# Kernel tuning notes

Measured on AMD Instinct MI355X. Metric: run time of the kernel, lower is better.

Reference implementation:

```python
import jax, jax.numpy as jnp
import numpy as np

HIDDEN = 128
GRID = 8
NB = 32.0            # neighborhood_size
CELL = NB / GRID      # cell_size


def setup_inputs() -> dict:
    key = jax.random.key(0)
    k1, k2, k3, k4 = jax.random.split(key, 4)
    N = 1024
    hidden_states = jax.random.normal(k1, (N, HIDDEN), dtype=jnp.float32)
    positions = jax.random.uniform(k2, (N, 2), dtype=jnp.float32) * 100.0
    fan_in = GRID * GRID * HIDDEN
    bound = 1.0 / np.sqrt(fan_in)
    W = jax.random.uniform(k3, (fan_in, HIDDEN), dtype=jnp.float32, minval=-bound, maxval=bound)
    b = jax.random.uniform(k4, (HIDDEN,), dtype=jnp.float32, minval=-bound, maxval=bound)
    return {"hidden_states": hidden_states, "positions": positions, "W": W, "b": b}


def reference(hidden_states, positions, W, b):
    N, H = hidden_states.shape
    G = GRID
    pos = jax.lax.stop_gradient(positions)  # indices carry no gradient (matches torch int())
    # rel[i, j] = positions[j] - positions[i]
    rel = pos[None, :, :] - pos[:, None, :]                      # [N, N, 2]
    half = NB / 2.0
    inside = (jnp.abs(rel[..., 0]) <= half) & (jnp.abs(rel[..., 1]) <= half)
    not_self = ~jnp.eye(N, dtype=bool)
    valid = inside & not_self                                     # [N, N]
    # rel + half is in [0, NB] when inside, so floor == int() truncation
    gx = jnp.clip(jnp.floor((rel[..., 0] + half) / CELL).astype(jnp.int32), 0, G - 1)
    gy = jnp.clip(jnp.floor((rel[..., 1] + half) / CELL).astype(jnp.int32), 0, G - 1)
    cell = gy * G + gx                                            # [N, N], in [0, G*G)
    # invalid pairs go to a dummy cell G*G per pedestrian
    seg = jnp.where(valid, cell, G * G)
    gid = (jnp.arange(N, dtype=jnp.int32)[:, None] * (G * G + 1) + seg).reshape(-1)
    data = jnp.broadcast_to(hidden_states[None, :, :], (N, N, H)).reshape(N * N, H)
    gmax = jax.ops.segment_max(data, gid, num_segments=N * (G * G + 1))  # [N*(G*G+1), H]
    # torch grid starts at zeros and uses maximum -> clamp at 0; empty cells (-inf) -> 0
    grid = jnp.maximum(gmax.reshape(N, G * G + 1, H)[:, : G * G, :], 0.0)  # [N, G*G, H]
    flat = grid.reshape(N, G * G * H)
    return flat @ W + b
```

## Files before the change

### kernel.cpp

```cpp
#include <hip/hip_runtime.h>
#include <hip/hip_bf16.h>

#define N_PED 1024
#define H 128
#define G 8
#define NCELL 64
#define K_TOT 8192
#define HALF_NB 16.0f
#define INV_CELL 0.25f

#define KSPLIT 16
#define KC 512
#define BM 32
#define BK 64
#define NSTAGE 8

typedef __attribute__((ext_vector_type(8))) short bf16x8;
typedef __attribute__((ext_vector_type(4))) float f32x4;

__device__ __forceinline__ unsigned map_f2u(float v) {
    unsigned u = __float_as_uint(v);
    return (u & 0x80000000u) ? ~u : (u | 0x80000000u);
}
__device__ __forceinline__ float unmap_u2f(unsigned u) {
    return __uint_as_float((u & 0x80000000u) ? (u ^ 0x80000000u) : ~u);
}
__device__ __forceinline__ unsigned pack2(unsigned ua, unsigned ub) {
    float2 f = {unmap_u2f(ua), unmap_u2f(ub)};
    union { __hip_bfloat162 h; unsigned u; } cv;
    cv.h = __float22bfloat162_rn(f);
    return cv.u;
}
__device__ __forceinline__ unsigned pack2f(float fa, float fb) {
    float2 f = {fa, fb};
    union { __hip_bfloat162 h; unsigned u; } cv;
    cv.h = __float22bfloat162_rn(f);
    return cv.u;
}
__device__ __forceinline__ void gl_lds16(const void* g, void* l) {
    __builtin_amdgcn_global_load_lds(
        (const __attribute__((address_space(1))) void*)g,
        (__attribute__((address_space(3))) void*)l, 16, 0, 0);
}

__global__ __launch_bounds__(512) void fused_pre(const float* __restrict__ hs,
                                                 const float* __restrict__ pos,
                                                 const float* __restrict__ W,
                                                 const float* __restrict__ b,
                                                 ushort* __restrict__ grid,
                                                 ushort* __restrict__ Wt,
                                                 float* __restrict__ out) {
    __shared__ __align__(16) char smem[36872];
    const int tid = threadIdx.x;

    if (blockIdx.x < N_PED) {
        unsigned* lgrid = (unsigned*)smem;
        int*      list  = (int*)(smem + 32768);
        int*      cnt   = (int*)(smem + 36864);
        const int i = blockIdx.x;

        const unsigned iu = 0x80000000u;
        uint4 iv = {iu, iu, iu, iu};
        for (int k = tid; k < NCELL * H / 4; k += 512) ((uint4*)lgrid)[k] = iv;
        if (tid == 0) *cnt = 0;
        __syncthreads();

        const float2 pi = ((const float2*)pos)[i];
        for (int j = tid; j < N_PED; j += 512) {
            float2 pj = ((const float2*)pos)[j];
            float rx = pj.x - pi.x;
            float ry = pj.y - pi.y;
            if (j != i && fabsf(rx) <= HALF_NB && fabsf(ry) <= HALF_NB) {
                int gx = min(G - 1, max(0, (int)floorf((rx + HALF_NB) * INV_CELL)));
                int gy = min(G - 1, max(0, (int)floorf((ry + HALF_NB) * INV_CELL)));
                int slot = atomicAdd(cnt, 1);
                list[slot] = (j << 8) | (gy * G + gx);
            }
        }
        __syncthreads();

        const int n  = *cnt;
        const int c  = tid & 31;
        const int eg = tid >> 5;
        int e  = eg;
        int p0 = (e < n) ? list[e] : -1;
        int p1 = (e + 16 < n) ? list[e + 16] : -1;
        float v0[4] = {};
        if (p0 >= 0) {
            const float* hp = &hs[(p0 >> 8) * H + c];
            v0[0] = hp[0]; v0[1] = hp[32]; v0[2] = hp[64]; v0[3] = hp[96];
        }
        while (p0 >= 0) {
            int p2 = (e + 32 < n) ? list[e + 32] : -1;
            float v1[4] = {};
            if (p1 >= 0) {
                const float* hp = &hs[(p1 >> 8) * H + c];
                v1[0] = hp[0]; v1[1] = hp[32]; v1[2] = hp[64]; v1[3] = hp[96];
            }
            unsigned* gph = &lgrid[(p0 & 255) * H + c];
            atomicMax(gph + 0,  map_f2u(v0[0]));
            atomicMax(gph + 32, map_f2u(v0[1]));
            atomicMax(gph + 64, map_f2u(v0[2]));
            atomicMax(gph + 96, map_f2u(v0[3]));
            e += 16; p0 = p1; p1 = p2;
            v0[0] = v1[0]; v0[1] = v1[1]; v0[2] = v1[2]; v0[3] = v1[3];
        }
        __syncthreads();

        uint4* dst = (uint4*)(grid + (size_t)i * K_TOT);
        for (int q = tid; q < K_TOT / 8; q += 512) {
            uint4 a  = ((const uint4*)lgrid)[2 * q];
            uint4 bq = ((const uint4*)lgrid)[2 * q + 1];
            uint4 o;
            o.x = pack2(a.x,  a.y);
            o.y = pack2(a.z,  a.w);
            o.z = pack2(bq.x, bq.y);
            o.w = pack2(bq.z, bq.w);
            dst[q] = o;
        }
    } else if (blockIdx.x < N_PED + 128) {
        float* tile = (float*)smem;
        const int bw  = blockIdx.x - N_PED;
        const int k0w = bw * 64;

        for (int x = tid; x < 64 * H; x += 512) {
            int r = x >> 7, cc = x & 127;
            tile[r * 129 + cc] = W[(size_t)(k0w + r) * H + cc];
        }
        __syncthreads();

        const int col = tid >> 2;
        const int kh  = (tid & 3) * 16;
        uint tmp[8];
        #pragma unroll
        for (int t = 0; t < 8; ++t)
            tmp[t] = pack2f(tile[(kh + 2 * t) * 129 + col],
                            tile[(kh + 2 * t + 1) * 129 + col]);
        uint4* w0 = (uint4*)(Wt + (size_t)col * K_TOT + k0w + kh);
        w0[0] = *(const uint4*)&tmp[0];
        w0[1] = *(const uint4*)&tmp[4];
    } else {
        const float4* b4 = (const float4*)b;
        float4* out4 = (float4*)out;
        const int b0 = (blockIdx.x - N_PED - 128) * 16384;
        for (int i2 = tid; i2 < 16384; i2 += 512) {
            int g = b0 + i2;
            out4[g] = b4[g & 31];
        }
    }
}

__global__ __launch_bounds__(256) void gemm_mfma(const ushort* __restrict__ A,
                                                 const ushort* __restrict__ Wt,
                                                 float* __restrict__ out) {
    __shared__ ushort sA[3][BM * BK];
    __shared__ ushort sB[3][H * BK];

    const int m0   = blockIdx.x * BM;
    const int k0   = blockIdx.y * KC;
    const int tid  = threadIdx.x;
    const int wave = tid >> 6;
    const int lane = tid & 63;
    const int ll   = lane & 15;
    const int lh   = lane >> 4;
    const int lr8  = lane >> 3;
    const int cswz = (lane & 7) ^ (lr8 & 7);

    const ushort* Abase = A  + (size_t)(m0 + 8 * wave + lr8) * K_TOT + k0 + cswz * 8;
    const ushort* Bbase = Wt + (size_t)(32 * wave + lr8) * K_TOT      + k0 + cswz * 8;

    f32x4 acc[2][2] = {};

#define STAGE(T, BUF)                                                        \
    do {                                                                     \
        gl_lds16(Abase + (T) * BK, &sA[BUF][8 * wave * BK]);                 \
        gl_lds16(Bbase + (T) * BK,                &sB[BUF][(32 * wave) * BK]);      \
        gl_lds16(Bbase + (T) * BK +  8 * K_TOT,   &sB[BUF][(32 * wave + 8) * BK]);  \
        gl_lds16(Bbase + (T) * BK + 16 * K_TOT,   &sB[BUF][(32 * wave + 16) * BK]); \
        gl_lds16(Bbase + (T) * BK + 24 * K_TOT,   &sB[BUF][(32 * wave + 24) * BK]); \
    } while (0)

    STAGE(0, 0);
    STAGE(1, 1);
    asm volatile("s_waitcnt vmcnt(5)" ::: "memory");
    __builtin_amdgcn_s_barrier();

    #pragma unroll
    for (int t = 0; t < NSTAGE; ++t) {
        if (t + 2 < NSTAGE) STAGE(t + 2, (t + 2) % 3);

        const int buf = t % 3;
        #pragma unroll
        for (int ks = 0; ks < 2; ++ks) {
            const int chunk = ks * 4 + lh;
            bf16x8 bfrag[2], afrag[2];
            #pragma unroll
            for (int nt = 0; nt < 2; ++nt) {
                int br = wave * 32 + nt * 16 + ll;
                bfrag[nt] = *(const bf16x8*)&sB[buf][br * BK + ((chunk ^ (br & 7)) * 8)];
            }
            #pragma unroll
            for (int mt = 0; mt < 2; ++mt) {
                int ar = mt * 16 + ll;
                afrag[mt] = *(const bf16x8*)&sA[buf][ar * BK + ((chunk ^ (ar & 7)) * 8)];
            }
            #pragma unroll
            for (int mt = 0; mt < 2; ++mt)
                #pragma unroll
                for (int nt = 0; nt < 2; ++nt)
                    acc[mt][nt] = __builtin_amdgcn_mfma_f32_16x16x32_bf16(
                        afrag[mt], bfrag[nt], acc[mt][nt], 0, 0, 0);
        }

        if (t + 1 < NSTAGE) {
            if (t + 2 < NSTAGE)
                asm volatile("s_waitcnt vmcnt(5)" ::: "memory");
            else
                asm volatile("s_waitcnt vmcnt(0)" ::: "memory");
            __builtin_amdgcn_s_barrier();
        }
    }
#undef STAGE

    #pragma unroll
    for (int mt = 0; mt < 2; ++mt)
        #pragma unroll
        for (int nt = 0; nt < 2; ++nt) {
            int col   = wave * 32 + nt * 16 + ll;
            int rbase = m0 + mt * 16 + lh * 4;
            #pragma unroll
            for (int r = 0; r < 4; ++r)
                atomicAdd(&out[(size_t)(rbase + r) * H + col], acc[mt][nt][r]);
        }
}

extern "C" void kernel_launch(void* const* d_in, const int* in_sizes, int n_in,
                              void* d_out, int out_size, void* d_ws, size_t ws_size,
                              hipStream_t stream) {
    const float* hs  = (const float*)d_in[0];
    const float* pos = (const float*)d_in[1];
    const float* Wm  = (const float*)d_in[2];
    const float* b   = (const float*)d_in[3];
    float* out = (float*)d_out;

    ushort* grid = (ushort*)d_ws;
    ushort* Wt   = (ushort*)((char*)d_ws + (16u << 20));

    fused_pre<<<N_PED + 128 + 2, 512, 0, stream>>>(hs, pos, Wm, b, grid, Wt, out);
    gemm_mfma<<<dim3(N_PED / BM, KSPLIT), 256, 0, stream>>>(grid, Wt, out);
}
```

Measured before the change: 33.24 us.

## Replace atomic split-K accumulation with partial buffers and a separate reduce kernel

```diff
diff --git a/kernel.cpp b/kernel.cpp
--- a/kernel.cpp
+++ b/kernel.cpp
@@ -11,7 +11,7 @@
 
 #define KSPLIT 16
 #define KC 512
-#define BM 32
+#define BM 64
 #define BK 64
 #define NSTAGE 8
 
@@ -46,10 +46,8 @@
 __global__ __launch_bounds__(512) void fused_pre(const float* __restrict__ hs,
                                                  const float* __restrict__ pos,
                                                  const float* __restrict__ W,
-                                                 const float* __restrict__ b,
                                                  ushort* __restrict__ grid,
-                                                 ushort* __restrict__ Wt,
-                                                 float* __restrict__ out) {
+                                                 ushort* __restrict__ Wt) {
     __shared__ __align__(16) char smem[36872];
     const int tid = threadIdx.x;
 
@@ -118,7 +116,7 @@
             o.w = pack2(bq.z, bq.w);
             dst[q] = o;
         }
-    } else if (blockIdx.x < N_PED + 128) {
+    } else {
         float* tile = (float*)smem;
         const int bw  = blockIdx.x - N_PED;
         const int k0w = bw * 64;
@@ -139,20 +137,12 @@
         uint4* w0 = (uint4*)(Wt + (size_t)col * K_TOT + k0w + kh);
         w0[0] = *(const uint4*)&tmp[0];
         w0[1] = *(const uint4*)&tmp[4];
-    } else {
-        const float4* b4 = (const float4*)b;
-        float4* out4 = (float4*)out;
-        const int b0 = (blockIdx.x - N_PED - 128) * 16384;
-        for (int i2 = tid; i2 < 16384; i2 += 512) {
-            int g = b0 + i2;
-            out4[g] = b4[g & 31];
-        }
     }
 }
 
-__global__ __launch_bounds__(256) void gemm_mfma(const ushort* __restrict__ A,
+__global__ __launch_bounds__(512) void gemm_mfma(const ushort* __restrict__ A,
                                                  const ushort* __restrict__ Wt,
-                                                 float* __restrict__ out) {
+                                                 float* __restrict__ part) {
     __shared__ ushort sA[3][BM * BK];
     __shared__ ushort sB[3][H * BK];
 
@@ -165,24 +155,24 @@
     const int lh   = lane >> 4;
     const int lr8  = lane >> 3;
     const int cswz = (lane & 7) ^ (lr8 & 7);
+    const int wr   = wave >> 2;
+    const int wc   = wave & 3;
 
     const ushort* Abase = A  + (size_t)(m0 + 8 * wave + lr8) * K_TOT + k0 + cswz * 8;
-    const ushort* Bbase = Wt + (size_t)(32 * wave + lr8) * K_TOT      + k0 + cswz * 8;
+    const ushort* Bbase = Wt + (size_t)(16 * wave + lr8) * K_TOT     + k0 + cswz * 8;
 
     f32x4 acc[2][2] = {};
 
-#define STAGE(T, BUF)                                                        \
-    do {                                                                     \
-        gl_lds16(Abase + (T) * BK, &sA[BUF][8 * wave * BK]);                 \
-        gl_lds16(Bbase + (T) * BK,                &sB[BUF][(32 * wave) * BK]);      \
-        gl_lds16(Bbase + (T) * BK +  8 * K_TOT,   &sB[BUF][(32 * wave + 8) * BK]);  \
-        gl_lds16(Bbase + (T) * BK + 16 * K_TOT,   &sB[BUF][(32 * wave + 16) * BK]); \
-        gl_lds16(Bbase + (T) * BK + 24 * K_TOT,   &sB[BUF][(32 * wave + 24) * BK]); \
+#define STAGE(T, BUF)                                                          \
+    do {                                                                       \
+        gl_lds16(Abase + (T) * BK, &sA[BUF][(8 * wave) * BK]);                 \
+        gl_lds16(Bbase + (T) * BK,              &sB[BUF][(16 * wave) * BK]);   \
+        gl_lds16(Bbase + (T) * BK + 8 * K_TOT,  &sB[BUF][(16 * wave + 8) * BK]); \
     } while (0)
 
     STAGE(0, 0);
     STAGE(1, 1);
-    asm volatile("s_waitcnt vmcnt(5)" ::: "memory");
+    asm volatile("s_waitcnt vmcnt(3)" ::: "memory");
     __builtin_amdgcn_s_barrier();
 
     #pragma unroll
@@ -192,17 +182,17 @@
         const int buf = t % 3;
         #pragma unroll
         for (int ks = 0; ks < 2; ++ks) {
-            const int chunk = ks * 4 + lh;
-            bf16x8 bfrag[2], afrag[2];
+            const int ch = ks * 4 + lh;
+            bf16x8 afrag[2], bfrag[2];
+            #pragma unroll
+            for (int mt = 0; mt < 2; ++mt) {
+                int ar = wr * 32 + mt * 16 + ll;
+                afrag[mt] = *(const bf16x8*)&sA[buf][ar * BK + ((ch ^ (ar & 7)) * 8)];
+            }
             #pragma unroll
             for (int nt = 0; nt < 2; ++nt) {
-                int br = wave * 32 + nt * 16 + ll;
-                bfrag[nt] = *(const bf16x8*)&sB[buf][br * BK + ((chunk ^ (br & 7)) * 8)];
-            }
-            #pragma unroll
-            for (int mt = 0; mt < 2; ++mt) {
-                int ar = mt * 16 + ll;
-                afrag[mt] = *(const bf16x8*)&sA[buf][ar * BK + ((chunk ^ (ar & 7)) * 8)];
+                int br = wc * 32 + nt * 16 + ll;
+                bfrag[nt] = *(const bf16x8*)&sB[buf][br * BK + ((ch ^ (br & 7)) * 8)];
             }
             #pragma unroll
             for (int mt = 0; mt < 2; ++mt)
@@ -214,7 +204,7 @@
 
         if (t + 1 < NSTAGE) {
             if (t + 2 < NSTAGE)
-                asm volatile("s_waitcnt vmcnt(5)" ::: "memory");
+                asm volatile("s_waitcnt vmcnt(3)" ::: "memory");
             else
                 asm volatile("s_waitcnt vmcnt(0)" ::: "memory");
             __builtin_amdgcn_s_barrier();
@@ -222,16 +212,30 @@
     }
 #undef STAGE
 
+    float* dst = part + (size_t)blockIdx.y * (N_PED * H);
     #pragma unroll
     for (int mt = 0; mt < 2; ++mt)
         #pragma unroll
         for (int nt = 0; nt < 2; ++nt) {
-            int col   = wave * 32 + nt * 16 + ll;
-            int rbase = m0 + mt * 16 + lh * 4;
+            int col   = wc * 32 + nt * 16 + ll;
+            int rbase = m0 + wr * 32 + mt * 16 + lh * 4;
             #pragma unroll
             for (int r = 0; r < 4; ++r)
-                atomicAdd(&out[(size_t)(rbase + r) * H + col], acc[mt][nt][r]);
-        }
+                dst[(size_t)(rbase + r) * H + col] = acc[mt][nt][r];
+        }
+}
+
+__global__ __launch_bounds__(128) void reduce_out(const float* __restrict__ part,
+                                                  const float* __restrict__ b,
+                                                  float* __restrict__ out) {
+    const int idx = (blockIdx.x * 128 + threadIdx.x) * 4;
+    float4 acc = *(const float4*)&b[idx & (H - 1)];
+    #pragma unroll
+    for (int s = 0; s < KSPLIT; ++s) {
+        float4 p = *(const float4*)&part[(size_t)s * (N_PED * H) + idx];
+        acc.x += p.x; acc.y += p.y; acc.z += p.z; acc.w += p.w;
+    }
+    *(float4*)&out[idx] = acc;
 }
 
 extern "C" void kernel_launch(void* const* d_in, const int* in_sizes, int n_in,
@@ -245,7 +249,9 @@
 
     ushort* grid = (ushort*)d_ws;
     ushort* Wt   = (ushort*)((char*)d_ws + (16u << 20));
-
-    fused_pre<<<N_PED + 128 + 2, 512, 0, stream>>>(hs, pos, Wm, b, grid, Wt, out);
-    gemm_mfma<<<dim3(N_PED / BM, KSPLIT), 256, 0, stream>>>(grid, Wt, out);
-}
+    float*  part = (float*)((char*)d_ws + (18u << 20));
+
+    fused_pre<<<N_PED + 128, 512, 0, stream>>>(hs, pos, Wm, grid, Wt);
+    gemm_mfma<<<dim3(N_PED / BM, KSPLIT), 512, 0, stream>>>(grid, Wt, part);
+    reduce_out<<<(N_PED * H) / (128 * 4), 128, 0, stream>>>(part, b, out);
+}
```

Result: faster. 28.77 us (-13.5%).
